# Kernel tuning notes

Hardware: AMD Instinct MI355X
Metric: run time of the kernel (lower is better)

Reference implementation:

```python
import jax, jax.numpy as jnp
import numpy as np

NUM_HEADS = 16
NUM_GROUPS = 4
NUM_KV_HEADS = NUM_HEADS // NUM_GROUPS  # 4
HEAD_DIM = 64
MAX_DIST = 484


def setup_inputs() -> dict:
    key = jax.random.key(0)
    ks = jax.random.split(key, 8)
    B, S, E, H = 32, 484, 1024, 1024
    kv_dim = HEAD_DIM * NUM_GROUPS  # 256
    s_in = 0.03
    return {
        "query": jax.random.normal(ks[0], (B, S, E), dtype=jnp.float32),
        "key": jax.random.normal(ks[1], (B, S, E), dtype=jnp.float32),
        "value": jax.random.normal(ks[2], (B, S, E), dtype=jnp.float32),
        "Wq": jax.random.normal(ks[3], (E, H), dtype=jnp.float32) * s_in,
        "Wk": jax.random.normal(ks[4], (E, kv_dim), dtype=jnp.float32) * s_in,
        "Wv": jax.random.normal(ks[5], (E, kv_dim), dtype=jnp.float32) * s_in,
        "Wo": jax.random.normal(ks[6], (H, E), dtype=jnp.float32) * s_in,
        "rel_table": jax.random.normal(ks[7], (2 * MAX_DIST - 1, NUM_HEADS), dtype=jnp.float32) * 0.02,
    }


def _rel_bias(rel_table, q_len, k_len):
    # relative position k - q, clipped to [-(MD-1), MD-1], shifted to table index
    rel = jnp.arange(k_len)[None, :] - jnp.arange(q_len)[:, None]
    idx = jnp.clip(rel, -(MAX_DIST - 1), MAX_DIST - 1) + (MAX_DIST - 1)
    bias = rel_table[idx]  # [q, k, heads]
    return jnp.transpose(bias, (2, 0, 1))  # [heads, q, k]


def reference(query, key, value, Wq, Wk, Wv, Wo, rel_table):
    B, Q, _ = query.shape
    K = key.shape[1]
    G, Hkv, D = NUM_GROUPS, NUM_KV_HEADS, HEAD_DIM
    # projections; torch head split: head index = g*Hkv + h
    q = (query @ Wq).reshape(B, Q, G * Hkv, D).transpose(0, 2, 1, 3)
    q = q.reshape(B, G, Hkv, Q, D)  # b g h sq d
    k = (key @ Wk).reshape(B, K, G, D).transpose(0, 2, 1, 3)  # b g sk d
    v = (value @ Wv).reshape(B, K, G, D).transpose(0, 2, 1, 3)  # b g sv d
    scale = jnp.float32(D) ** 0.5
    scores = jnp.einsum('bghqd,bgkd->bghqk', q, k) / scale
    bias = _rel_bias(rel_table, Q, K).reshape(1, G, Hkv, Q, K)
    attn = jax.nn.softmax(scores + bias, axis=-1)
    out = jnp.einsum('bghqk,bgkd->bghqd', attn, v)
    out = out.reshape(B, G * Hkv, Q, D).transpose(0, 2, 1, 3).reshape(B, Q, G * Hkv * D)
    return out @ Wo
```

## Files before the change

### kernel.cpp

```cpp
#include <hip/hip_runtime.h>
#include <hip/hip_bf16.h>

typedef __attribute__((ext_vector_type(8))) short short8;
typedef __attribute__((ext_vector_type(4))) float f32x4;
typedef __attribute__((ext_vector_type(4))) unsigned uintx4;

#define B_  32
#define S_  484
#define E_  1024
#define NH  16
#define SP  512
#define M_  (B_*S_)

static __device__ __forceinline__ ushort f2bf(float f) {
  union { float f; unsigned u; } v; v.f = f;
  unsigned u = v.u;
  return (ushort)((u + 0x7FFFu + ((u >> 16) & 1u)) >> 16);
}

static __device__ __forceinline__ unsigned cvt_pk_bf16(float lo, float hi) {
  unsigned r;
  asm("v_cvt_pk_bf16_f32 %0, %1, %2" : "=v"(r) : "v"(lo), "v"(hi));
  return r;
}

#define GLOAD_LDS16(gp, lp) \
  __builtin_amdgcn_global_load_lds((const __attribute__((address_space(1))) void*)(gp), \
                                   (__attribute__((address_space(3))) void*)(lp), 16, 0, 0)

__global__ __launch_bounds__(256)
void prep_all(const float* __restrict__ Wq, const float* __restrict__ Wk,
              const float* __restrict__ Wv, const float* __restrict__ Wo,
              ushort* __restrict__ wqT, ushort* __restrict__ wkT,
              ushort* __restrict__ wvT, ushort* __restrict__ woT,
              const float* __restrict__ query, ushort* __restrict__ qb, int n4) {
  if (blockIdx.x >= 2560) {
    int i = (blockIdx.x - 2560) * 256 + threadIdx.x;
    int stride = 2048 * 256;
    for (; i < n4; i += stride) {
      float4 v = ((const float4*)query)[i];
      ushort4 h;
      h.x = f2bf(v.x); h.y = f2bf(v.y); h.z = f2bf(v.z); h.w = f2bf(v.w);
      ((ushort4*)qb)[i] = h;
    }
    return;
  }
  __shared__ float tile[32][33];
  int t = blockIdx.x;
  const float* W; ushort* WT; int N;
  if (t < 1024)      { W = Wq; WT = wqT; N = 1024; }
  else if (t < 1280) { W = Wk; WT = wkT; N = 256;  t -= 1024; }
  else if (t < 1536) { W = Wv; WT = wvT; N = 256;  t -= 1280; }
  else               { W = Wo; WT = woT; N = 1024; t -= 1536; }
  const int nx = N >> 5;
  const int n0 = (t % nx) * 32, k0 = (t / nx) * 32;
  const int tx = threadIdx.x & 31, ty = threadIdx.x >> 5;
  for (int i = ty; i < 32; i += 8) tile[i][tx] = W[(size_t)(k0 + i) * N + n0 + tx];
  __syncthreads();
  for (int i = ty; i < 32; i += 8) WT[(size_t)(n0 + i) * 1024 + k0 + tx] = f2bf(tile[tx][i]);
}

template<int EPI>
__global__ __launch_bounds__(512)
void gemm_cnt256(const ushort* __restrict__ A, const ushort* __restrict__ BT,
                 void* __restrict__ Cout, float oscale) {
  const int K = 1024, N = 1024, NK = 32;
  __shared__ alignas(16) ushort sA[4][256 * 32];
  __shared__ alignas(16) ushort sB[4][256 * 32];
  const int tid = threadIdx.x;
  const int lane = tid & 63, w = tid >> 6;

  const int nwg = gridDim.x;
  const int qq = nwg >> 3, rr = nwg & 7;
  const int x = blockIdx.x & 7, seq = blockIdx.x >> 3;
  const int logical = x * qq + (x < rr ? x : rr) + seq;
  const int m0 = (logical >> 2) * 256;
  const int n0 = (logical & 3) * 256;

  const int brow = tid >> 2;
  const int scol = (((tid & 3) ^ ((tid >> 3) & 3))) * 8;
  const int rowA0 = min(m0 + brow, M_ - 1);
  const int rowA1 = min(m0 + brow + 128, M_ - 1);
  const ushort* gA0 = A + (size_t)rowA0 * K + scol;
  const ushort* gA1 = A + (size_t)rowA1 * K + scol;
  const ushort* gB0 = BT + (size_t)(n0 + brow) * K + scol;
  const int dst = tid * 8;

  const int wr = w >> 2, wc = w & 3;
  const int g4 = lane >> 4, l16 = lane & 15;
  const int rs = (l16 >> 1) & 3;

  f32x4 acc[8][4] = {};

  auto stage = [&](int kt, int buf) {
    GLOAD_LDS16(gA0 + kt * 32,           &sA[buf][dst]);
    GLOAD_LDS16(gA1 + kt * 32,           &sA[buf][dst + 4096]);
    GLOAD_LDS16(gB0 + kt * 32,           &sB[buf][dst]);
    GLOAD_LDS16(gB0 + kt * 32 + 128 * K, &sB[buf][dst + 4096]);
  };

  stage(0, 0);
  stage(1, 1);
  stage(2, 2);

  int cur = 0;
  for (int kt = 0; kt < NK; ++kt) {
    if (kt < NK - 2)       asm volatile("s_waitcnt vmcnt(8)" ::: "memory");
    else if (kt == NK - 2) asm volatile("s_waitcnt vmcnt(4)" ::: "memory");
    else                   asm volatile("s_waitcnt vmcnt(0)" ::: "memory");
    asm volatile("s_waitcnt lgkmcnt(0)" ::: "memory");
    __builtin_amdgcn_s_barrier();
    if (kt + 3 < NK) stage(kt + 3, (cur + 3) & 3);
    const ushort* pa = &sA[cur][(wr * 128 + l16) * 32 + 8 * (g4 ^ rs)];
    const ushort* pb = &sB[cur][(wc * 64 + l16) * 32 + 8 * (g4 ^ rs)];
    short8 af[8], bf[4];
#pragma unroll
    for (int i = 0; i < 8; ++i) af[i] = *(const short8*)(pa + i * 16 * 32);
#pragma unroll
    for (int i = 0; i < 4; ++i) bf[i] = *(const short8*)(pb + i * 16 * 32);
#pragma unroll
    for (int mi = 0; mi < 8; ++mi)
#pragma unroll
      for (int ni = 0; ni < 4; ++ni)
        acc[mi][ni] = __builtin_amdgcn_mfma_f32_16x16x32_bf16(af[mi], bf[ni], acc[mi][ni], 0, 0, 0);
    cur = (cur + 1) & 3;
  }

#pragma unroll
  for (int mi = 0; mi < 8; ++mi) {
#pragma unroll
    for (int ni = 0; ni < 4; ++ni) {
#pragma unroll
      for (int r = 0; r < 4; ++r) {
        int m = m0 + wr * 128 + mi * 16 + g4 * 4 + r;
        int n = n0 + wc * 64 + ni * 16 + l16;
        if (m < M_) {
          float vv = acc[mi][ni][r];
          if (EPI == 2) {
            ((float*)Cout)[(size_t)m * N + n] = vv;
          } else {
            int b = m / S_, pos = m % S_;
            ushort hv = f2bf(vv * oscale);
            ((ushort*)Cout)[(((size_t)b * NH + (n >> 6)) * SP + pos) * 64 + (n & 63)] = hv;
          }
        }
      }
    }
  }
}

__global__ __launch_bounds__(512, 2)
void kvproj256(const float* __restrict__ key, const float* __restrict__ value,
               const ushort* __restrict__ BT,
               ushort* __restrict__ kp, ushort* __restrict__ vp) {
  const int K = 1024, NK = 32;
  __shared__ alignas(16) ushort sA[4][256 * 32];
  __shared__ alignas(16) ushort sB[4][128 * 32];
  const int tid = threadIdx.x;
  const int lane = tid & 63, w = tid >> 6;

  const int nwg = gridDim.x;
  const int qq = nwg >> 3, rr = nwg & 7;
  const int x = blockIdx.x & 7, seq = blockIdx.x >> 3;
  const int logical = x * qq + (x < rr ? x : rr) + seq;
  const int m0 = (logical >> 2) * 256;
  const int sub = logical & 3;
  const bool isV = sub >= 2;
  const int n0l = (sub & 1) * 128;
  const float* Ain = isV ? value : key;

  const int brow = tid >> 2;
  const int scol = (((tid & 3) ^ ((tid >> 3) & 3))) * 8;
  const ushort* gB0 = BT + (size_t)((isV ? 256 : 0) + n0l + brow) * K + scol;
  const int dstB = tid * 8;

  const int arow = tid >> 1;
  const int rowAf = min(m0 + arow, M_ - 1);
  const float* gAf = Ain + (size_t)rowAf * K + (tid & 1) * 16;
  const int sw = (arow >> 1) & 3;
  const int ag0 = (2 * (tid & 1)) ^ sw;
  const int ag1 = (2 * (tid & 1) + 1) ^ sw;

  const int wr = w >> 1, wc = w & 1;
  const int g4 = lane >> 4, l16 = lane & 15;
  const int rs = (l16 >> 1) & 3;

  f32x4 acc[4][4] = {};
  float4 fA[3][4];

  auto stageB = [&](int kt) {
    GLOAD_LDS16(gB0 + kt * 32, &sB[kt & 3][dstB]);
  };
  auto compute = [&](int kt) {
    const int buf = kt & 3;
    const ushort* pa = &sA[buf][(wr * 64 + l16) * 32 + 8 * (g4 ^ rs)];
    const ushort* pb = &sB[buf][(wc * 64 + l16) * 32 + 8 * (g4 ^ rs)];
    short8 af[4], bf[4];
#pragma unroll
    for (int i = 0; i < 4; ++i) {
      af[i] = *(const short8*)(pa + i * 16 * 32);
      bf[i] = *(const short8*)(pb + i * 16 * 32);
    }
#pragma unroll
    for (int mi = 0; mi < 4; ++mi)
#pragma unroll
      for (int ni = 0; ni < 4; ++ni)
        acc[mi][ni] = __builtin_amdgcn_mfma_f32_16x16x32_bf16(af[mi], bf[ni], acc[mi][ni], 0, 0, 0);
  };

#define ISSUEA(kt, slot) do { \
    const float4* _p = (const float4*)(gAf + (kt) * 32); \
    fA[slot][0] = _p[0]; fA[slot][1] = _p[1]; fA[slot][2] = _p[2]; fA[slot][3] = _p[3]; \
  } while (0)
#define WRITEA(kt, slot) do { \
    unsigned _d0 = cvt_pk_bf16(fA[slot][0].x, fA[slot][0].y), _d1 = cvt_pk_bf16(fA[slot][0].z, fA[slot][0].w); \
    unsigned _d2 = cvt_pk_bf16(fA[slot][1].x, fA[slot][1].y), _d3 = cvt_pk_bf16(fA[slot][1].z, fA[slot][1].w); \
    unsigned _d4 = cvt_pk_bf16(fA[slot][2].x, fA[slot][2].y), _d5 = cvt_pk_bf16(fA[slot][2].z, fA[slot][2].w); \
    unsigned _d6 = cvt_pk_bf16(fA[slot][3].x, fA[slot][3].y), _d7 = cvt_pk_bf16(fA[slot][3].z, fA[slot][3].w); \
    ushort* _base = &sA[(kt) & 3][arow * 32]; \
    uintx4 _q0 = {_d0, _d1, _d2, _d3}, _q1 = {_d4, _d5, _d6, _d7}; \
    *(uintx4*)(_base + ag0 * 8) = _q0; \
    *(uintx4*)(_base + ag1 * 8) = _q1; \
  } while (0)
#define KSTEP(kt, ws, is) do { \
    if ((kt) < NK - 2) asm volatile("s_waitcnt vmcnt(5)" ::: "memory"); \
    else               asm volatile("s_waitcnt vmcnt(0)" ::: "memory"); \
    if ((kt) + 1 < NK) WRITEA((kt) + 1, ws); \
    asm volatile("s_waitcnt lgkmcnt(0)" ::: "memory"); \
    __builtin_amdgcn_s_barrier(); \
    if ((kt) + 3 < NK) { stageB((kt) + 3); ISSUEA((kt) + 3, is); } \
    compute(kt); \
  } while (0)

  stageB(0); ISSUEA(0, 0);
  stageB(1); ISSUEA(1, 1);
  stageB(2); ISSUEA(2, 2);
  asm volatile("s_waitcnt vmcnt(10)" ::: "memory");
  WRITEA(0, 0);

  for (int kb = 0; kb < 30; kb += 3) {
    KSTEP(kb,     1, 0);
    KSTEP(kb + 1, 2, 1);
    KSTEP(kb + 2, 0, 2);
  }
  KSTEP(30, 1, 0);
  KSTEP(31, 0, 0);

#undef KSTEP
#undef WRITEA
#undef ISSUEA

#pragma unroll
  for (int mi = 0; mi < 4; ++mi) {
#pragma unroll
    for (int ni = 0; ni < 4; ++ni) {
#pragma unroll
      for (int r = 0; r < 4; ++r) {
        int m = m0 + wr * 64 + mi * 16 + g4 * 4 + r;
        int nl = n0l + wc * 64 + ni * 16 + l16;
        if (m < M_) {
          float vv = acc[mi][ni][r];
          int b = m / S_, pos = m % S_;
          int h = nl >> 6, d = nl & 63;
          if (!isV) {
            int dd = d ^ ((pos & 7) << 3);
            kp[(((size_t)b * 4 + h) * SP + pos) * 64 + dd] = f2bf(vv);
          } else {
            int local = pos & 31;
            int j = (local < 16) ? (2 * local) : (2 * local - 31);
            int pf_ = (pos & ~31) | (j ^ ((d & 3) << 3));
            vp[(((size_t)b * 4 + h) * 64 + d) * SP + pf_] = f2bf(vv);
          }
        }
      }
    }
  }
}

__global__ __launch_bounds__(256)
void attn_kernel(const ushort* __restrict__ qp, const ushort* __restrict__ kp,
                 const ushort* __restrict__ vpT, const float* __restrict__ rel,
                 ushort* __restrict__ ao) {
  __shared__ float2 sBiasP[640];
  __shared__ alignas(16) ushort sK[2][32 * 64];
  __shared__ alignas(16) ushort sV[2][64 * 32];
  __shared__ alignas(16) ushort sP[4][32 * 40];
  const int tid = threadIdx.x;
  const int blk = blockIdx.x;
  const int logical = (blk & 7) * 256 + (blk >> 3);
  const int qt = logical & 3, head = (logical >> 2) & 15, b = logical >> 6;
  const int g = head >> 2;
  const float LOG2E = 1.44269504f;
  const int tbase = 384 - qt * 128;
  for (int t = tid; t < 640; t += 256) {
    int gi0 = t + tbase - 32;
    int gi1 = t + tbase - 16;
    float b0 = (gi0 >= 0 && gi0 < 967) ? rel[gi0 * 16 + head] * LOG2E : -1e30f;
    float b1 = (gi1 >= 0 && gi1 < 967) ? rel[gi1 * 16 + head] * LOG2E : -1e30f;
    sBiasP[t] = make_float2(b0, b1);
  }

  const int lane = tid & 63, w = tid >> 6;
  const int g4 = lane >> 4, l16 = lane & 15;
  const int qw = qt * 128 + w * 32;

  const ushort* qbA = qp + (((size_t)b * NH + head) * SP + qw + l16) * 64;
  const ushort* qbB = qbA + 16 * 64;
  short8 qf0a = *(const short8*)(qbA + 8 * g4);
  short8 qf1a = *(const short8*)(qbA + 32 + 8 * g4);
  short8 qf0b = *(const short8*)(qbB + 8 * g4);
  short8 qf1b = *(const short8*)(qbB + 32 + 8 * g4);

  const ushort* kSrc = kp  + ((size_t)b * 4 + g) * SP * 64 + (tid >> 3) * 64 + (tid & 7) * 8;
  const ushort* vSrc = vpT + ((size_t)b * 4 + g) * 64 * SP + (tid >> 2) * SP + (tid & 3) * 8;

  f32x4 accA[4] = {}, accB[4] = {};
  float psA[4] = {0.f, 0.f, 0.f, 0.f}, psB[4] = {0.f, 0.f, 0.f, 0.f};
  const int ibA = l16 - (w * 32 + g4 * 4) + 131;
  const int ibB = ibA - 16;
  ushort* sPw = &sP[w][0];

  const int kswz  = (l16 & 7) << 3;
  const int kOff0 = l16 * 64 + ((8 * g4) ^ kswz);
  const int kOff1 = l16 * 64 + ((32 + 8 * g4) ^ kswz);
  const int vOff  = l16 * 32 + 8 * (g4 ^ (l16 & 3));

  GLOAD_LDS16(kSrc, &sK[0][w * 512]);
  GLOAD_LDS16(vSrc, &sV[0][w * 512]);

  for (int kt = 0; kt < 16; ++kt) {
    __syncthreads();
    if (kt + 1 < 16) {
      GLOAD_LDS16(kSrc + (kt + 1) * 2048, &sK[(kt + 1) & 1][w * 512]);
      GLOAD_LDS16(vSrc + (kt + 1) * 32,   &sV[(kt + 1) & 1][w * 512]);
    }
    const int k0 = kt * 32;
    float2 a0 = sBiasP[ibA + k0],     a1 = sBiasP[ibA + k0 - 1];
    float2 a2 = sBiasP[ibA + k0 - 2], a3 = sBiasP[ibA + k0 - 3];
    float2 c0 = sBiasP[ibB + k0],     c1 = sBiasP[ibB + k0 - 1];
    float2 c2 = sBiasP[ibB + k0 - 2], c3 = sBiasP[ibB + k0 - 3];
    f32x4 s0a = {a0.x, a1.x, a2.x, a3.x}, s1a = {a0.y, a1.y, a2.y, a3.y};
    f32x4 s0b = {c0.x, c1.x, c2.x, c3.x}, s1b = {c0.y, c1.y, c2.y, c3.y};

    const ushort* sk = &sK[kt & 1][0];
    const ushort* sv = &sV[kt & 1][0];
    short8 kf0 = *(const short8*)(sk + kOff0);
    short8 kf1 = *(const short8*)(sk + kOff1);
    short8 kf2 = *(const short8*)(sk + 1024 + kOff0);
    short8 kf3 = *(const short8*)(sk + 1024 + kOff1);
    s0a = __builtin_amdgcn_mfma_f32_16x16x32_bf16(qf0a, kf0, s0a, 0, 0, 0);
    s0a = __builtin_amdgcn_mfma_f32_16x16x32_bf16(qf1a, kf1, s0a, 0, 0, 0);
    s1a = __builtin_amdgcn_mfma_f32_16x16x32_bf16(qf0a, kf2, s1a, 0, 0, 0);
    s1a = __builtin_amdgcn_mfma_f32_16x16x32_bf16(qf1a, kf3, s1a, 0, 0, 0);
    s0b = __builtin_amdgcn_mfma_f32_16x16x32_bf16(qf0b, kf0, s0b, 0, 0, 0);
    s0b = __builtin_amdgcn_mfma_f32_16x16x32_bf16(qf1b, kf1, s0b, 0, 0, 0);
    s1b = __builtin_amdgcn_mfma_f32_16x16x32_bf16(qf0b, kf2, s1b, 0, 0, 0);
    s1b = __builtin_amdgcn_mfma_f32_16x16x32_bf16(qf1b, kf3, s1b, 0, 0, 0);

#pragma unroll
    for (int r = 0; r < 4; ++r) {
      float p0 = __builtin_amdgcn_exp2f(s0a[r]);
      float p1 = __builtin_amdgcn_exp2f(s1a[r]);
      float u0 = __builtin_amdgcn_exp2f(s0b[r]);
      float u1 = __builtin_amdgcn_exp2f(s1b[r]);
      if (kt == 15) {
        bool m0v = (k0 + l16 < S_), m1v = (k0 + 16 + l16 < S_);
        p0 = m0v ? p0 : 0.f;  p1 = m1v ? p1 : 0.f;
        u0 = m0v ? u0 : 0.f;  u1 = m1v ? u1 : 0.f;
      }
      psA[r] += p0 + p1;
      psB[r] += u0 + u1;
      *(unsigned*)(sPw + (g4 * 4 + r) * 40 + 2 * l16)        = cvt_pk_bf16(p0, p1);
      *(unsigned*)(sPw + (16 + g4 * 4 + r) * 40 + 2 * l16)   = cvt_pk_bf16(u0, u1);
    }
    short8 pfA = *(const short8*)(sPw + l16 * 40 + 8 * g4);
    short8 pfB = *(const short8*)(sPw + (16 + l16) * 40 + 8 * g4);
#pragma unroll
    for (int nt = 0; nt < 4; ++nt) {
      short8 vf = *(const short8*)(sv + vOff + nt * 512);
      accA[nt] = __builtin_amdgcn_mfma_f32_16x16x32_bf16(pfA, vf, accA[nt], 0, 0, 0);
      accB[nt] = __builtin_amdgcn_mfma_f32_16x16x32_bf16(pfB, vf, accB[nt], 0, 0, 0);
    }
  }

#pragma unroll
  for (int off = 1; off < 16; off <<= 1) {
#pragma unroll
    for (int r = 0; r < 4; ++r) {
      psA[r] += __shfl_xor(psA[r], off, 64);
      psB[r] += __shfl_xor(psB[r], off, 64);
    }
  }

#pragma unroll
  for (int r = 0; r < 4; ++r) {
    int qa = qw + g4 * 4 + r;
    if (qa < S_) {
      float inv = 1.f / psA[r];
#pragma unroll
      for (int nt = 0; nt < 4; ++nt)
        ao[((size_t)b * S_ + qa) * 1024 + head * 64 + nt * 16 + l16] = f2bf(accA[nt][r] * inv);
    }
    int qb2 = qa + 16;
    if (qb2 < S_) {
      float inv = 1.f / psB[r];
#pragma unroll
      for (int nt = 0; nt < 4; ++nt)
        ao[((size_t)b * S_ + qb2) * 1024 + head * 64 + nt * 16 + l16] = f2bf(accB[nt][r] * inv);
    }
  }
}

extern "C" void kernel_launch(void* const* d_in, const int* in_sizes, int n_in,
                              void* d_out, int out_size, void* d_ws, size_t ws_size,
                              hipStream_t stream) {
  const float* query = (const float*)d_in[0];
  const float* key   = (const float*)d_in[1];
  const float* value = (const float*)d_in[2];
  const float* Wq    = (const float*)d_in[3];
  const float* Wk    = (const float*)d_in[4];
  const float* Wv    = (const float*)d_in[5];
  const float* Wo    = (const float*)d_in[6];
  const float* rel   = (const float*)d_in[7];

  char* ws = (char*)d_ws;
  size_t off = 0;
  auto alloc = [&](size_t bytes) { char* p = ws + off; off += (bytes + 255) & ~(size_t)255; return p; };

  const size_t MEelems = (size_t)M_ * E_;
  ushort* qb  = (ushort*)alloc(MEelems * 2);
  ushort* wqT = (ushort*)alloc((size_t)1024 * 1024 * 2);
  ushort* wkT = (ushort*)alloc((size_t)256 * 1024 * 2);
  ushort* wvT = (ushort*)alloc((size_t)256 * 1024 * 2);
  ushort* woT = (ushort*)alloc((size_t)1024 * 1024 * 2);
  ushort* qp  = (ushort*)alloc((size_t)B_ * NH * SP * 64 * 2);
  ushort* kp  = (ushort*)alloc((size_t)B_ * 4 * SP * 64 * 2);
  ushort* vp  = (ushort*)alloc((size_t)B_ * 4 * 64 * SP * 2);
  ushort* ao  = (ushort*)alloc(MEelems * 2);
  (void)wvT;

  prep_all<<<4608, 256, 0, stream>>>(Wq, Wk, Wv, Wo, wqT, wkT, wvT, woT,
                                     query, qb, (int)(MEelems / 4));

  const float QSCALE = 0.125f * 1.44269504f;
  gemm_cnt256<0><<<244, 512, 0, stream>>>(qb, wqT, qp, QSCALE);
  kvproj256<<<244, 512, 0, stream>>>(key, value, wkT, kp, vp);

  attn_kernel<<<2048, 256, 0, stream>>>(qp, kp, vp, rel, ao);

  gemm_cnt256<2><<<244, 512, 0, stream>>>(ao, woT, d_out, 1.0f);
}
```

Measured before the change: 253.4 us.

## Pre-convert key/value to bf16 in prep kernel and load via LDS DMA

Key and value activations are now converted to bf16 in the prep kernel alongside query, so the K/V projection kernel can stage its A operand directly into LDS with global_load_lds instead of loading fp32 into registers and converting on the fly. This removes register pressure and the conversion and LDS-write work from the projection's inner loop, and drops the two-blocks-per-CU launch bound. In exchange it writes and then re-reads two extra bf16 activation buffers, adding global memory traffic. The V layout swizzle is also changed, both in the projection epilogue and in the attention kernel's read offset, to alter the LDS bank pattern.

```diff
diff --git a/kernel.cpp b/kernel.cpp
--- a/kernel.cpp
+++ b/kernel.cpp
@@ -33,15 +33,22 @@
               const float* __restrict__ Wv, const float* __restrict__ Wo,
               ushort* __restrict__ wqT, ushort* __restrict__ wkT,
               ushort* __restrict__ wvT, ushort* __restrict__ woT,
-              const float* __restrict__ query, ushort* __restrict__ qb, int n4) {
+              const float* __restrict__ query, const float* __restrict__ key,
+              const float* __restrict__ value,
+              ushort* __restrict__ qb, ushort* __restrict__ kb,
+              ushort* __restrict__ vb, int n4) {
   if (blockIdx.x >= 2560) {
-    int i = (blockIdx.x - 2560) * 256 + threadIdx.x;
-    int stride = 2048 * 256;
-    for (; i < n4; i += stride) {
-      float4 v = ((const float4*)query)[i];
-      ushort4 h;
-      h.x = f2bf(v.x); h.y = f2bf(v.y); h.z = f2bf(v.z); h.w = f2bf(v.w);
-      ((ushort4*)qb)[i] = h;
+    const int base = (blockIdx.x - 2560) * 256 + threadIdx.x;
+    const int stride = 2048 * 256;
+    for (int j = 0; j < 3; ++j) {
+      const float* src = (j == 0) ? query : (j == 1) ? key : value;
+      ushort* dst = (j == 0) ? qb : (j == 1) ? kb : vb;
+      for (int i = base; i < n4; i += stride) {
+        float4 v = ((const float4*)src)[i];
+        ushort4 h;
+        h.x = f2bf(v.x); h.y = f2bf(v.y); h.z = f2bf(v.z); h.w = f2bf(v.w);
+        ((ushort4*)dst)[i] = h;
+      }
     }
     return;
   }
@@ -149,8 +156,8 @@
   }
 }
 
-__global__ __launch_bounds__(512, 2)
-void kvproj256(const float* __restrict__ key, const float* __restrict__ value,
+__global__ __launch_bounds__(512)
+void kvproj_bf(const ushort* __restrict__ kb, const ushort* __restrict__ vb,
                const ushort* __restrict__ BT,
                ushort* __restrict__ kp, ushort* __restrict__ vp) {
   const int K = 1024, NK = 32;
@@ -167,34 +174,43 @@
   const int sub = logical & 3;
   const bool isV = sub >= 2;
   const int n0l = (sub & 1) * 128;
-  const float* Ain = isV ? value : key;
+  const ushort* Ain = isV ? vb : kb;
 
   const int brow = tid >> 2;
   const int scol = (((tid & 3) ^ ((tid >> 3) & 3))) * 8;
+  const int rowA0 = min(m0 + brow, M_ - 1);
+  const int rowA1 = min(m0 + brow + 128, M_ - 1);
+  const ushort* gA0 = Ain + (size_t)rowA0 * K + scol;
+  const ushort* gA1 = Ain + (size_t)rowA1 * K + scol;
   const ushort* gB0 = BT + (size_t)((isV ? 256 : 0) + n0l + brow) * K + scol;
-  const int dstB = tid * 8;
-
-  const int arow = tid >> 1;
-  const int rowAf = min(m0 + arow, M_ - 1);
-  const float* gAf = Ain + (size_t)rowAf * K + (tid & 1) * 16;
-  const int sw = (arow >> 1) & 3;
-  const int ag0 = (2 * (tid & 1)) ^ sw;
-  const int ag1 = (2 * (tid & 1) + 1) ^ sw;
+  const int dst = tid * 8;
 
   const int wr = w >> 1, wc = w & 1;
   const int g4 = lane >> 4, l16 = lane & 15;
   const int rs = (l16 >> 1) & 3;
 
   f32x4 acc[4][4] = {};
-  float4 fA[3][4];
-
-  auto stageB = [&](int kt) {
-    GLOAD_LDS16(gB0 + kt * 32, &sB[kt & 3][dstB]);
+
+  auto stage = [&](int kt, int buf) {
+    GLOAD_LDS16(gA0 + kt * 32, &sA[buf][dst]);
+    GLOAD_LDS16(gA1 + kt * 32, &sA[buf][dst + 4096]);
+    GLOAD_LDS16(gB0 + kt * 32, &sB[buf][dst]);
   };
-  auto compute = [&](int kt) {
-    const int buf = kt & 3;
-    const ushort* pa = &sA[buf][(wr * 64 + l16) * 32 + 8 * (g4 ^ rs)];
-    const ushort* pb = &sB[buf][(wc * 64 + l16) * 32 + 8 * (g4 ^ rs)];
+
+  stage(0, 0);
+  stage(1, 1);
+  stage(2, 2);
+
+  int cur = 0;
+  for (int kt = 0; kt < NK; ++kt) {
+    if (kt < NK - 2)       asm volatile("s_waitcnt vmcnt(6)" ::: "memory");
+    else if (kt == NK - 2) asm volatile("s_waitcnt vmcnt(3)" ::: "memory");
+    else                   asm volatile("s_waitcnt vmcnt(0)" ::: "memory");
+    asm volatile("s_waitcnt lgkmcnt(0)" ::: "memory");
+    __builtin_amdgcn_s_barrier();
+    if (kt + 3 < NK) stage(kt + 3, (cur + 3) & 3);
+    const ushort* pa = &sA[cur][(wr * 64 + l16) * 32 + 8 * (g4 ^ rs)];
+    const ushort* pb = &sB[cur][(wc * 64 + l16) * 32 + 8 * (g4 ^ rs)];
     short8 af[4], bf[4];
 #pragma unroll
     for (int i = 0; i < 4; ++i) {
@@ -206,49 +222,8 @@
 #pragma unroll
       for (int ni = 0; ni < 4; ++ni)
         acc[mi][ni] = __builtin_amdgcn_mfma_f32_16x16x32_bf16(af[mi], bf[ni], acc[mi][ni], 0, 0, 0);
-  };
-
-#define ISSUEA(kt, slot) do { \
-    const float4* _p = (const float4*)(gAf + (kt) * 32); \
-    fA[slot][0] = _p[0]; fA[slot][1] = _p[1]; fA[slot][2] = _p[2]; fA[slot][3] = _p[3]; \
-  } while (0)
-#define WRITEA(kt, slot) do { \
-    unsigned _d0 = cvt_pk_bf16(fA[slot][0].x, fA[slot][0].y), _d1 = cvt_pk_bf16(fA[slot][0].z, fA[slot][0].w); \
-    unsigned _d2 = cvt_pk_bf16(fA[slot][1].x, fA[slot][1].y), _d3 = cvt_pk_bf16(fA[slot][1].z, fA[slot][1].w); \
-    unsigned _d4 = cvt_pk_bf16(fA[slot][2].x, fA[slot][2].y), _d5 = cvt_pk_bf16(fA[slot][2].z, fA[slot][2].w); \
-    unsigned _d6 = cvt_pk_bf16(fA[slot][3].x, fA[slot][3].y), _d7 = cvt_pk_bf16(fA[slot][3].z, fA[slot][3].w); \
-    ushort* _base = &sA[(kt) & 3][arow * 32]; \
-    uintx4 _q0 = {_d0, _d1, _d2, _d3}, _q1 = {_d4, _d5, _d6, _d7}; \
-    *(uintx4*)(_base + ag0 * 8) = _q0; \
-    *(uintx4*)(_base + ag1 * 8) = _q1; \
-  } while (0)
-#define KSTEP(kt, ws, is) do { \
-    if ((kt) < NK - 2) asm volatile("s_waitcnt vmcnt(5)" ::: "memory"); \
-    else               asm volatile("s_waitcnt vmcnt(0)" ::: "memory"); \
-    if ((kt) + 1 < NK) WRITEA((kt) + 1, ws); \
-    asm volatile("s_waitcnt lgkmcnt(0)" ::: "memory"); \
-    __builtin_amdgcn_s_barrier(); \
-    if ((kt) + 3 < NK) { stageB((kt) + 3); ISSUEA((kt) + 3, is); } \
-    compute(kt); \
-  } while (0)
-
-  stageB(0); ISSUEA(0, 0);
-  stageB(1); ISSUEA(1, 1);
-  stageB(2); ISSUEA(2, 2);
-  asm volatile("s_waitcnt vmcnt(10)" ::: "memory");
-  WRITEA(0, 0);
-
-  for (int kb = 0; kb < 30; kb += 3) {
-    KSTEP(kb,     1, 0);
-    KSTEP(kb + 1, 2, 1);
-    KSTEP(kb + 2, 0, 2);
-  }
-  KSTEP(30, 1, 0);
-  KSTEP(31, 0, 0);
-
-#undef KSTEP
-#undef WRITEA
-#undef ISSUEA
+    cur = (cur + 1) & 3;
+  }
 
 #pragma unroll
   for (int mi = 0; mi < 4; ++mi) {
@@ -268,7 +243,7 @@
           } else {
             int local = pos & 31;
             int j = (local < 16) ? (2 * local) : (2 * local - 31);
-            int pf_ = (pos & ~31) | (j ^ ((d & 3) << 3));
+            int pf_ = (pos & ~31) | (j ^ (((d >> 1) & 3) << 3));
             vp[(((size_t)b * 4 + h) * 64 + d) * SP + pf_] = f2bf(vv);
           }
         }
@@ -323,7 +298,7 @@
   const int kswz  = (l16 & 7) << 3;
   const int kOff0 = l16 * 64 + ((8 * g4) ^ kswz);
   const int kOff1 = l16 * 64 + ((32 + 8 * g4) ^ kswz);
-  const int vOff  = l16 * 32 + 8 * (g4 ^ (l16 & 3));
+  const int vOff  = l16 * 32 + 8 * (g4 ^ ((l16 >> 1) & 3));
 
   GLOAD_LDS16(kSrc, &sK[0][w * 512]);
   GLOAD_LDS16(vSrc, &sV[0][w * 512]);
@@ -429,6 +404,8 @@
 
   const size_t MEelems = (size_t)M_ * E_;
   ushort* qb  = (ushort*)alloc(MEelems * 2);
+  ushort* kb  = (ushort*)alloc(MEelems * 2);
+  ushort* vb  = (ushort*)alloc(MEelems * 2);
   ushort* wqT = (ushort*)alloc((size_t)1024 * 1024 * 2);
   ushort* wkT = (ushort*)alloc((size_t)256 * 1024 * 2);
   ushort* wvT = (ushort*)alloc((size_t)256 * 1024 * 2);
@@ -440,11 +417,11 @@
   (void)wvT;
 
   prep_all<<<4608, 256, 0, stream>>>(Wq, Wk, Wv, Wo, wqT, wkT, wvT, woT,
-                                     query, qb, (int)(MEelems / 4));
+                                     query, key, value, qb, kb, vb, (int)(MEelems / 4));
 
   const float QSCALE = 0.125f * 1.44269504f;
   gemm_cnt256<0><<<244, 512, 0, stream>>>(qb, wqT, qp, QSCALE);
-  kvproj256<<<244, 512, 0, stream>>>(key, value, wkT, kp, vp);
+  kvproj_bf<<<244, 512, 0, stream>>>(kb, vb, wkT, kp, vp);
 
   attn_kernel<<<2048, 256, 0, stream>>>(qp, kp, vp, rel, ao);
 
```

Result: slower. 271.5 us (+7.1%).
